# Kernel optimization log

Measured on AMD Instinct MI355X. Metric: run time of the kernel, lower is better.

## Reference

```python
import jax, jax.numpy as jnp
import numpy as np

B, SEQ, VOCAB, DIM, DEPTH, HEADS, DH, M, FF, LABELS = 4, 2048, 4096, 768, 6, 12, 64, 256, 3072, 2
INNER = HEADS * DH
EPS_K = 1e-4  # FAVOR+ kernel eps
EPS_LN = 1e-5


def setup_inputs() -> dict:
    key = jax.random.key(0)
    ks = jax.random.split(key, 16)
    g = lambda k, shape: (jax.random.normal(k, shape, jnp.float32) * 0.02)
    return {
        "x": jax.random.randint(ks[0], (B, SEQ), 0, VOCAB),
        "token_emb": g(ks[1], (VOCAB, DIM)),
        "pos_emb": g(ks[2], (SEQ, DIM)),
        "ln1_g": jnp.ones((DEPTH, DIM)), "ln1_b": jnp.zeros((DEPTH, DIM)),
        "Wq": g(ks[3], (DEPTH, DIM, INNER)),
        "Wk": g(ks[4], (DEPTH, DIM, INNER)),
        "Wv": g(ks[5], (DEPTH, DIM, INNER)),
        "Wo": g(ks[6], (DEPTH, INNER, DIM)), "bo": jnp.zeros((DEPTH, DIM)),
        "proj": jax.random.normal(ks[7], (DEPTH, M, DH), jnp.float32),  # FAVOR+ random projections (buffer)
        "ln2_g": jnp.ones((DEPTH, DIM)), "ln2_b": jnp.zeros((DEPTH, DIM)),
        "W1": g(ks[8], (DEPTH, DIM, FF)), "b1": jnp.zeros((DEPTH, FF)),
        "W2": g(ks[9], (DEPTH, FF, DIM)), "b2": jnp.zeros((DEPTH, DIM)),
        "lnf_g": jnp.ones((DIM,)), "lnf_b": jnp.zeros((DIM,)),
        "Wp": g(ks[10], (DIM, DIM)), "bp": jnp.zeros((DIM,)),
        "Wc": g(ks[11], (DIM, LABELS)), "bc": jnp.zeros((LABELS,)),
    }


def layernorm(x, g, b):
    mu = jnp.mean(x, -1, keepdims=True)
    var = jnp.mean(jnp.square(x - mu), -1, keepdims=True)
    return (x - mu) * jax.lax.rsqrt(var + EPS_LN) * g + b


def softmax_kernel(x, proj, is_query):
    # x: [b,h,n,d]  proj: [m,d]   (FAVOR+ positive softmax features)
    d = x.shape[-1]
    m = proj.shape[0]
    dn = d ** -0.25            # data normalizer 1/sqrt(sqrt(d))
    ratio = m ** -0.5
    xd = jnp.einsum('bhnd,md->bhnm', x * dn, proj)
    diag = 0.5 * jnp.sum(jnp.square(x), -1, keepdims=True) * (dn * dn)  # [b,h,n,1]
    if is_query:
        stab = jnp.max(xd, axis=-1, keepdims=True)
    else:
        stab = jnp.max(xd, axis=(-2, -1), keepdims=True)
    return ratio * (jnp.exp(xd - diag - stab) + EPS_K)


def favor_attention(y, Wq, Wk, Wv, Wo, bo, proj):
    b, n, _ = y.shape
    split = lambda t: t.reshape(b, n, HEADS, DH).transpose(0, 2, 1, 3)  # -> bhnd
    q, k, v = split(y @ Wq), split(y @ Wk), split(y @ Wv)
    qp = softmax_kernel(q, proj, True)    # [b,h,n,m]
    kp = softmax_kernel(k, proj, False)   # [b,h,n,m]
    k_sum = jnp.sum(kp, axis=2)                                  # [b,h,m]
    d_inv = 1.0 / jnp.einsum('bhnm,bhm->bhn', qp, k_sum)
    ctx = jnp.einsum('bhnm,bhnd->bhmd', kp, v)                   # [b,h,m,d]
    out = jnp.einsum('bhmd,bhnm,bhn->bhnd', ctx, qp, d_inv)
    out = out.transpose(0, 2, 1, 3).reshape(b, n, INNER)
    return out @ Wo + bo


def reference(x, token_emb, pos_emb, ln1_g, ln1_b, Wq, Wk, Wv, Wo, bo, proj,
              ln2_g, ln2_b, W1, b1, W2, b2, lnf_g, lnf_b, Wp, bp, Wc, bc):
    n = x.shape[1]
    h = token_emb[x] + pos_emb[None, :n]
    for l in range(DEPTH):
        h = h + favor_attention(layernorm(h, ln1_g[l], ln1_b[l]),
                                Wq[l], Wk[l], Wv[l], Wo[l], bo[l], proj[l])
        y = layernorm(h, ln2_g[l], ln2_b[l])
        h = h + (jax.nn.gelu(y @ W1[l] + b1[l], approximate=False) @ W2[l] + b2[l])
    h = layernorm(h, lnf_g, lnf_b)
    pooled = jnp.tanh(h[:, 0] @ Wp + bp)   # BertPooler on first token
    return pooled @ Wc + bc                 # [B, LABELS]
```

## Files before the change

kernel.cpp:

```cpp
#include <hip/hip_runtime.h>
#include <hip/hip_bf16.h>
#include <math.h>

#define B_ 4
#define SEQ_ 2048
#define DIM_ 768
#define DEPTH_ 6
#define HEADS_ 12
#define DH_ 64
#define MF_ 256
#define FF_ 3072
#define ROWS_ 8192
#define BH_ 48
#define QKVW_ 2304
#define DN_ 0.3535533905932738f
#define RATIO_ 0.0625f
#define EPSK_ 1e-4f
#define EPSLN_ 1e-5f

typedef unsigned short u16;
typedef unsigned int   u32;
typedef __bf16 bf16x8 __attribute__((ext_vector_type(8)));
typedef u16    u16x8  __attribute__((ext_vector_type(8)));
typedef float  f32x4  __attribute__((ext_vector_type(4)));

__device__ inline u16 f2bf(float x){
  u32 u = __builtin_bit_cast(u32, x);
  return (u16)((u + 0x7FFFu + ((u>>16)&1u)) >> 16);
}
__device__ inline float bf2f(u16 v){ return __builtin_bit_cast(float, (u32)v<<16); }

__device__ inline void gload16(const u16* g, u16* lds){
  __builtin_amdgcn_global_load_lds(
    (const __attribute__((address_space(1))) u32*)(const void*)g,
    (__attribute__((address_space(3))) u32*)(void*)lds, 16, 0, 0);
}

__global__ void embed_kernel(const int* __restrict__ x, const float4* __restrict__ tok,
                             const float4* __restrict__ pos, float4* __restrict__ h){
  const int C4 = DIM_/4;
  long total = (long)ROWS_*C4;
  for (long i = (long)blockIdx.x*blockDim.x + threadIdx.x; i < total;
       i += (long)gridDim.x*blockDim.x){
    int row = (int)(i / C4); int c = (int)(i - (long)row*C4);
    int n = row & (SEQ_-1);
    float4 a = tok[(long)x[row]*C4 + c];
    float4 p = pos[(long)n*C4 + c];
    float4 o; o.x=a.x+p.x; o.y=a.y+p.y; o.z=a.z+p.z; o.w=a.w+p.w;
    h[i] = o;
  }
}

__global__ __launch_bounds__(256) void ln_kernel(const float* __restrict__ X,
                          const float* __restrict__ g, const float* __restrict__ bta,
                          u16* __restrict__ Y){
  int row = blockIdx.x; int t = threadIdx.x;
  const float* xr = X + (long)row*DIM_;
  float v0 = xr[t], v1 = xr[t+256], v2 = xr[t+512];
  float s = v0+v1+v2;
  float ss = v0*v0+v1*v1+v2*v2;
  int lane = t&63, wid = t>>6;
  #pragma unroll
  for (int off=32; off; off>>=1){ s += __shfl_xor(s,off); ss += __shfl_xor(ss,off); }
  __shared__ float red[8];
  if (lane==0){ red[wid]=s; red[4+wid]=ss; }
  __syncthreads();
  s  = red[0]+red[1]+red[2]+red[3];
  ss = red[4]+red[5]+red[6]+red[7];
  float mu  = s*(1.0f/DIM_);
  float var = ss*(1.0f/DIM_) - mu*mu;
  float rs  = rsqrtf(var + EPSLN_);
  u16* yr = Y + (long)row*DIM_;
  yr[t]     = f2bf((v0-mu)*rs*g[t]     + bta[t]);
  yr[t+256] = f2bf((v1-mu)*rs*g[t+256] + bta[t+256]);
  yr[t+512] = f2bf((v2-mu)*rs*g[t+512] + bta[t+512]);
}

__global__ __launch_bounds__(256) void tconv_kernel(const float* __restrict__ W,
        u16* __restrict__ WT, int K, int N){
  __shared__ float tile[32][33];
  int n0 = blockIdx.x*32, k0 = blockIdx.y*32;
  int tx = threadIdx.x & 31, ty = threadIdx.x >> 5;
  #pragma unroll
  for (int i=0;i<32;i+=8) tile[ty+i][tx] = W[(long)(k0+ty+i)*N + n0+tx];
  __syncthreads();
  #pragma unroll
  for (int i=0;i<32;i+=8) WT[(long)(n0+ty+i)*K + k0+tx] = f2bf(tile[tx][ty+i]);
}

__global__ __launch_bounds__(256) void tconv4_kernel(const float* __restrict__ Wq,
        const float* __restrict__ Wk, const float* __restrict__ Wv,
        const float* __restrict__ Wo, u16* __restrict__ dst){
  __shared__ float tile[32][33];
  int z = blockIdx.z;
  const float* W = (z==0)?Wq:(z==1)?Wk:(z==2)?Wv:Wo;
  u16* WT = dst + (long)z*589824;
  int n0 = blockIdx.x*32, k0 = blockIdx.y*32;
  int tx = threadIdx.x & 31, ty = threadIdx.x >> 5;
  #pragma unroll
  for (int i=0;i<32;i+=8) tile[ty+i][tx] = W[(long)(k0+ty+i)*768 + n0+tx];
  __syncthreads();
  #pragma unroll
  for (int i=0;i<32;i+=8) WT[(long)(n0+ty+i)*768 + k0+tx] = f2bf(tile[tx][ty+i]);
}

template<int FM, int FN, int WM, int WN, int ACT, int CMODE, int BATCH>
__global__ __launch_bounds__(256) void mgemm(const u16* __restrict__ A,
     const u16* __restrict__ BT, const float* __restrict__ bias,
     void* __restrict__ Cv, const float* __restrict__ scale,
     int M, int N, int K, int ldC){
  (void)M;
  constexpr int BM = WM*FM*16, BN = WN*FN*16;
  constexpr int ACH = BM/16, BCH = BN/16;
  __shared__ u16 As[BM*32];
  __shared__ u16 Bs[BN*32];
  int tid = threadIdx.x; int w = tid>>6, l = tid&63;
  int bx, by;
  if (BATCH){ bx = blockIdx.x; by = blockIdx.y; }
  else {
    int bid = blockIdx.y*gridDim.x + blockIdx.x;
    int cpx = (gridDim.x*gridDim.y) >> 3;
    int swz = (bid & 7)*cpx + (bid >> 3);
    bx = swz % gridDim.x; by = swz / gridDim.x;
  }
  int m0 = by*BM, n0 = bx*BN;
  long coff = 0, srow0 = 0;
  if (BATCH){
    int z = blockIdx.z;
    A  += (long)z*2048*K;
    BT += (long)z*(long)N*K;
    coff  = (long)(z/HEADS_)*SEQ_*(long)ldC + (long)(z%HEADS_)*64;
    srow0 = (long)z*SEQ_;
  }
  f32x4 acc[FM][FN];
  #pragma unroll
  for (int i=0;i<FM;i++)
    #pragma unroll
    for (int j=0;j<FN;j++) acc[i][j] = (f32x4){0.f,0.f,0.f,0.f};

  const int row_l = l>>2, cq_l = l&3;
  const int wm = w / WN, wn = w % WN;
  const int kq = l>>4, rl15 = l&15;

  for (int k0=0; k0<K; k0+=32){
    __syncthreads();
    for (int c = w; c < ACH; c += 4){
      int r = c*16 + row_l;
      int gq = cq_l ^ ((r>>1)&3);
      gload16(A + (long)(m0+r)*K + k0 + gq*8, As + c*512);
    }
    for (int c = w; c < BCH; c += 4){
      int r = c*16 + row_l;
      int gq = cq_l ^ ((r>>1)&3);
      gload16(BT + (long)(n0+r)*K + k0 + gq*8, Bs + c*512);
    }
    __syncthreads();
    bf16x8 af[FM], bfr[FN];
    #pragma unroll
    for (int mi=0; mi<FM; mi++){
      int rr = (wm*FM + mi)*16 + rl15;
      int g = kq ^ ((rr>>1)&3);
      af[mi] = *(const bf16x8*)(As + rr*32 + g*8);
    }
    #pragma unroll
    for (int ni=0; ni<FN; ni++){
      int rr = (wn*FN + ni)*16 + rl15;
      int g = kq ^ ((rr>>1)&3);
      bfr[ni] = *(const bf16x8*)(Bs + rr*32 + g*8);
    }
    #pragma unroll
    for (int mi=0; mi<FM; mi++)
      #pragma unroll
      for (int ni=0; ni<FN; ni++)
        acc[mi][ni] = __builtin_amdgcn_mfma_f32_16x16x32_bf16(af[mi], bfr[ni], acc[mi][ni], 0, 0, 0);
  }

  int cc = l&15, rq = l>>4;
  #pragma unroll
  for (int mi=0; mi<FM; mi++){
    #pragma unroll
    for (int ni=0; ni<FN; ni++){
      int gcol = n0 + (wn*FN+ni)*16 + cc;
      float bv = bias ? bias[gcol] : 0.f;
      #pragma unroll
      for (int r4=0; r4<4; r4++){
        int grow = m0 + (wm*FM+mi)*16 + rq*4 + r4;
        float v = acc[mi][ni][r4] + bv;
        if (ACT) v = 0.5f*v*(1.0f + erff(v*0.70710678118654752f));
        if (CMODE==1){
          float* C = (float*)Cv;
          C[(long)grow*ldC + gcol] += v;
        } else if (CMODE==2){
          v *= scale[srow0 + grow];
          ((u16*)Cv)[coff + (long)grow*ldC + gcol] = f2bf(v);
        } else {
          ((u16*)Cv)[(long)grow*ldC + gcol] = f2bf(v);
        }
      }
    }
  }
}

__global__ void projcvt_kernel(const float* __restrict__ p, u16* __restrict__ hi,
                               u16* __restrict__ lo){
  int i = blockIdx.x*256 + threadIdx.x;
  float v = p[i];
  u16 h = f2bf(v);
  hi[i] = h;
  lo[i] = f2bf(v - bf2f(h));
}

__global__ __launch_bounds__(256) void diag2_kernel(const u16* __restrict__ qkvp,
        float* __restrict__ diagq, float* __restrict__ diagk){
  int chunk = blockIdx.x, z = blockIdx.y, which = blockIdx.z, t = threadIdx.x;
  const u16* X = qkvp + (which ? 768 : 0);
  float* outp = which ? diagk : diagq;
  int n = chunk*256 + t;
  const u16* r = X + ((long)(z/HEADS_)*SEQ_ + n)*QKVW_ + (z%HEADS_)*DH_;
  float s = 0.f;
  #pragma unroll
  for (int q=0;q<8;q++){
    u16x8 v = *(const u16x8*)(r + q*8);
    #pragma unroll
    for (int j=0;j<8;j++){ float f = bf2f(v[j]); s += f*f; }
  }
  outp[(long)z*SEQ_ + n] = 0.5f*DN_*DN_*s;
}

template<int MODE>
__global__ __launch_bounds__(256) void featgemm(const u16* __restrict__ X,
     const u16* __restrict__ PB, const float* __restrict__ diag,
     const float* __restrict__ stab, u16* __restrict__ kp,
     float* __restrict__ fmaxp){
  __shared__ u16 As[128*32];
  __shared__ u16 Bs[128*32];
  __shared__ float wred[4];
  int tid = threadIdx.x; int w = tid>>6, l = tid&63;
  int n0 = blockIdx.x*128, m0 = blockIdx.y*128;
  int z = blockIdx.z;
  const u16* A = X + (long)(z/HEADS_)*SEQ_*QKVW_ + (z%HEADS_)*DH_;
  f32x4 acc[4][4];
  #pragma unroll
  for (int i=0;i<4;i++)
    #pragma unroll
    for (int j=0;j<4;j++) acc[i][j] = (f32x4){0.f,0.f,0.f,0.f};
  const int row_l = l>>2, cq_l = l&3;
  const int wm = w>>1, wn = w&1;
  const int kq = l>>4, rl15 = l&15;

  for (int k0=0; k0<64; k0+=32){
    __syncthreads();
    for (int c = w; c < 8; c += 4){
      int r = c*16 + row_l;
      int gq = cq_l ^ ((r>>1)&3);
      gload16(A + (long)(m0+r)*QKVW_ + k0 + gq*8, As + c*512);
    }
    for (int c = w; c < 8; c += 4){
      int r = c*16 + row_l;
      int gq = cq_l ^ ((r>>1)&3);
      gload16(PB + (long)(n0+r)*64 + k0 + gq*8, Bs + c*512);
    }
    __syncthreads();
    bf16x8 af[4], bfr[4];
    #pragma unroll
    for (int mi=0; mi<4; mi++){
      int rr = (wm*4 + mi)*16 + rl15;
      int g = kq ^ ((rr>>1)&3);
      af[mi] = *(const bf16x8*)(As + rr*32 + g*8);
    }
    #pragma unroll
    for (int ni=0; ni<4; ni++){
      int rr = (wn*4 + ni)*16 + rl15;
      int g = kq ^ ((rr>>1)&3);
      bfr[ni] = *(const bf16x8*)(Bs + rr*32 + g*8);
    }
    #pragma unroll
    for (int mi=0; mi<4; mi++)
      #pragma unroll
      for (int ni=0; ni<4; ni++)
        acc[mi][ni] = __builtin_amdgcn_mfma_f32_16x16x32_bf16(af[mi], bfr[ni], acc[mi][ni], 0, 0, 0);
  }

  if (MODE==0){
    float bm = -1e30f;
    #pragma unroll
    for (int mi=0;mi<4;mi++)
      #pragma unroll
      for (int ni=0;ni<4;ni++)
        #pragma unroll
        for (int r4=0;r4<4;r4++) bm = fmaxf(bm, acc[mi][ni][r4]);
    bm *= DN_;
    #pragma unroll
    for (int off=32; off; off>>=1) bm = fmaxf(bm, __shfl_xor(bm,off));
    if (l==0) wred[w] = bm;
    __syncthreads();
    if (tid==0)
      fmaxp[z*32 + blockIdx.y*2 + blockIdx.x] =
        fmaxf(fmaxf(wred[0],wred[1]),fmaxf(wred[2],wred[3]));
  } else {
    float st = stab[z];
    int cc = l&15, rq = l>>4;
    #pragma unroll
    for (int mi=0; mi<4; mi++){
      #pragma unroll
      for (int ni=0; ni<4; ni++){
        int gcol = n0 + (wn*4+ni)*16 + cc;
        #pragma unroll
        for (int r4=0; r4<4; r4++){
          int grow = m0 + (wm*4+mi)*16 + rq*4 + r4;
          float v = acc[mi][ni][r4]*DN_;
          float e = RATIO_*(expf(v - diag[(long)z*SEQ_ + grow] - st) + EPSK_);
          kp[((long)z*SEQ_ + grow)*MF_ + gcol] = f2bf(e);
        }
      }
    }
  }
}

__global__ void fmax_reduce(const float* __restrict__ fmaxp, float* __restrict__ stab){
  int z = blockIdx.x, t = threadIdx.x;
  float m = (t<32) ? fmaxp[z*32+t] : -1e30f;
  #pragma unroll
  for (int off=32; off; off>>=1) m = fmaxf(m, __shfl_xor(m,off));
  if (t==0) stab[z] = m;
}

__global__ __launch_bounds__(256) void qfeatgemm(const u16* __restrict__ X,
     const u16* __restrict__ PH, const u16* __restrict__ PL,
     const float* __restrict__ diagq, const float* __restrict__ ksum,
     u16* __restrict__ qp, float* __restrict__ dinv){
  __shared__ u16 As[64*32];
  __shared__ u16 Bh[256*32];
  __shared__ u16 Bl[256*32];
  __shared__ float ksl[256];
  __shared__ float rmax[64][4];
  __shared__ float rsum[64][4];
  int tid = threadIdx.x; int w = tid>>6, l = tid&63;
  int n0 = blockIdx.x*64;
  int z = blockIdx.y;
  const u16* A = X + (long)(z/HEADS_)*SEQ_*QKVW_ + (z%HEADS_)*DH_;
  ksl[tid] = ksum[(long)z*MF_ + tid];
  f32x4 acc[4][4];
  #pragma unroll
  for (int i=0;i<4;i++)
    #pragma unroll
    for (int j=0;j<4;j++) acc[i][j] = (f32x4){0.f,0.f,0.f,0.f};
  const int row_l = l>>2, cq_l = l&3;
  const int kq = l>>4, rl15 = l&15;

  for (int k0=0; k0<64; k0+=32){
    __syncthreads();
    {
      int r = w*16 + row_l;
      int gq = cq_l ^ ((r>>1)&3);
      gload16(A + (long)(n0+r)*QKVW_ + k0 + gq*8, As + w*512);
    }
    for (int c = w; c < 16; c += 4){
      int r = c*16 + row_l;
      int gq = cq_l ^ ((r>>1)&3);
      gload16(PH + (long)r*64 + k0 + gq*8, Bh + c*512);
      gload16(PL + (long)r*64 + k0 + gq*8, Bl + c*512);
    }
    __syncthreads();
    bf16x8 af[4], bh[4], bl[4];
    #pragma unroll
    for (int mi=0; mi<4; mi++){
      int rr = mi*16 + rl15;
      int g = kq ^ ((rr>>1)&3);
      af[mi] = *(const bf16x8*)(As + rr*32 + g*8);
    }
    #pragma unroll
    for (int ni=0; ni<4; ni++){
      int rr = (w*4 + ni)*16 + rl15;
      int g = kq ^ ((rr>>1)&3);
      bh[ni] = *(const bf16x8*)(Bh + rr*32 + g*8);
      bl[ni] = *(const bf16x8*)(Bl + rr*32 + g*8);
    }
    #pragma unroll
    for (int mi=0; mi<4; mi++)
      #pragma unroll
      for (int ni=0; ni<4; ni++){
        acc[mi][ni] = __builtin_amdgcn_mfma_f32_16x16x32_bf16(af[mi], bh[ni], acc[mi][ni], 0, 0, 0);
        acc[mi][ni] = __builtin_amdgcn_mfma_f32_16x16x32_bf16(af[mi], bl[ni], acc[mi][ni], 0, 0, 0);
      }
  }

  int cc = l&15, rq = l>>4;
  #pragma unroll
  for (int mi=0; mi<4; mi++){
    #pragma unroll
    for (int r4=0; r4<4; r4++){
      float pm = fmaxf(fmaxf(acc[mi][0][r4],acc[mi][1][r4]),
                       fmaxf(acc[mi][2][r4],acc[mi][3][r4]));
      pm = fmaxf(pm, __shfl_xor(pm,1)); pm = fmaxf(pm, __shfl_xor(pm,2));
      pm = fmaxf(pm, __shfl_xor(pm,4)); pm = fmaxf(pm, __shfl_xor(pm,8));
      if (cc==0) rmax[mi*16 + rq*4 + r4][w] = pm;
    }
  }
  __syncthreads();
  #pragma unroll
  for (int mi=0; mi<4; mi++){
    #pragma unroll
    for (int r4=0; r4<4; r4++){
      int row = mi*16 + rq*4 + r4;
      float mx = fmaxf(fmaxf(rmax[row][0],rmax[row][1]),
                       fmaxf(rmax[row][2],rmax[row][3])) * DN_;
      float dq = diagq[(long)z*SEQ_ + n0 + row];
      float dv = 0.f;
      #pragma unroll
      for (int ni=0; ni<4; ni++){
        int col = w*64 + ni*16 + cc;
        float qpv = RATIO_*(expf(acc[mi][ni][r4]*DN_ - dq - mx) + EPSK_);
        u16 qb = f2bf(qpv);
        qp[((long)z*SEQ_ + n0 + row)*MF_ + col] = qb;
        dv += bf2f(qb)*ksl[col];
      }
      dv += __shfl_xor(dv,1); dv += __shfl_xor(dv,2);
      dv += __shfl_xor(dv,4); dv += __shfl_xor(dv,8);
      if (cc==0) rsum[row][w] = dv;
    }
  }
  __syncthreads();
  if (tid < 64){
    float s = rsum[tid][0]+rsum[tid][1]+rsum[tid][2]+rsum[tid][3];
    dinv[(long)z*SEQ_ + n0 + tid] = 1.0f/s;
  }
}

__global__ __launch_bounds__(256) void ctxgemm(const u16* __restrict__ qkv,
     const u16* __restrict__ kp, float* __restrict__ part){
  int kc = blockIdx.x;
  int z  = blockIdx.y;
  int b = z/HEADS_, hh = z%HEADS_;
  int tid = threadIdx.x; int w = tid>>6, l = tid&63;
  __shared__ u16 Vt[64*40];
  __shared__ u16 Kpt[256*40];
  f32x4 acc[4][4];
  #pragma unroll
  for (int i=0;i<4;i++)
    #pragma unroll
    for (int j=0;j<4;j++) acc[i][j] = (f32x4){0.f,0.f,0.f,0.f};
  int n_l = tid&31, grp = tid>>5;
  const int kq = l>>4, rl15 = l&15;
  const long vbase = (long)b*SEQ_*QKVW_ + hh*DH_ + 1536;
  const long kbase = (long)z*SEQ_*MF_;

  for (int s=0; s<32; s++){
    int nG = kc*1024 + s*32 + n_l;
    __syncthreads();
    {
      u16x8 v = *(const u16x8*)(qkv + vbase + (long)nG*QKVW_ + grp*8);
      #pragma unroll
      for (int j=0;j<8;j++) Vt[(grp*8+j)*40 + n_l] = v[j];
    }
    {
      const u16* src = kp + kbase + (long)nG*MF_ + grp*32;
      #pragma unroll
      for (int q=0;q<4;q++){
        u16x8 v = *(const u16x8*)(src + q*8);
        #pragma unroll
        for (int j=0;j<8;j++) Kpt[(grp*32+q*8+j)*40 + n_l] = v[j];
      }
    }
    __syncthreads();
    bf16x8 af[4], bfr[4];
    #pragma unroll
    for (int mi=0; mi<4; mi++)
      af[mi] = *(const bf16x8*)(Vt + (mi*16+rl15)*40 + kq*8);
    #pragma unroll
    for (int ni=0; ni<4; ni++)
      bfr[ni] = *(const bf16x8*)(Kpt + ((w*4+ni)*16+rl15)*40 + kq*8);
    #pragma unroll
    for (int mi=0; mi<4; mi++)
      #pragma unroll
      for (int ni=0; ni<4; ni++)
        acc[mi][ni] = __builtin_amdgcn_mfma_f32_16x16x32_bf16(af[mi], bfr[ni], acc[mi][ni], 0, 0, 0);
  }

  int cc = l&15, rq = l>>4;
  float* pb = part + ((long)kc*BH_ + z)*(64*MF_);
  #pragma unroll
  for (int mi=0; mi<4; mi++){
    #pragma unroll
    for (int ni=0; ni<4; ni++){
      int m = (w*4+ni)*16 + cc;
      #pragma unroll
      for (int r4=0; r4<4; r4++){
        int d = mi*16 + rq*4 + r4;
        pb[(long)d*MF_ + m] = acc[mi][ni][r4];
      }
    }
  }
}

__global__ void ctx_reduce2(const float* __restrict__ part, u16* __restrict__ ctxT){
  const long NT = (long)BH_*64*MF_;
  for (long i = (long)blockIdx.x*256 + threadIdx.x; i < NT; i += (long)gridDim.x*256){
    ctxT[i] = f2bf(part[i] + part[NT + i]);
  }
}

__global__ void ksum_part_kernel(const u16* __restrict__ kp, float* __restrict__ ksp){
  int kc = blockIdx.x, z = blockIdx.y, t = threadIdx.x;
  const u16* base = kp + ((long)z*SEQ_ + kc*256)*MF_ + t;
  float s = 0.f;
  for (int n=0;n<256;n++) s += bf2f(base[(long)n*MF_]);
  ksp[(z*8+kc)*MF_ + t] = s;
}

__global__ void ksum_reduce(const float* __restrict__ part, float* __restrict__ ksum){
  int z = blockIdx.x; int t = threadIdx.x;
  float s = 0.f;
  #pragma unroll
  for (int c=0;c<8;c++) s += part[(z*8+c)*MF_ + t];
  ksum[z*MF_+t] = s;
}

__global__ __launch_bounds__(256) void pooler_kernel(const float* __restrict__ h,
                           const float* __restrict__ g, const float* __restrict__ bta,
                           const float* __restrict__ Wp, const float* __restrict__ bp,
                           const float* __restrict__ Wc, const float* __restrict__ bc,
                           float* __restrict__ out){
  int b = blockIdx.x, t = threadIdx.x;
  __shared__ float xn[768];
  __shared__ float pl[768];
  __shared__ float red[8];
  const float* row = h + (long)b*SEQ_*DIM_;
  float v0=row[t], v1=row[t+256], v2=row[t+512];
  float s = v0+v1+v2, ss = v0*v0+v1*v1+v2*v2;
  int lane=t&63, wid=t>>6;
  #pragma unroll
  for (int off=32; off; off>>=1){ s += __shfl_xor(s,off); ss += __shfl_xor(ss,off); }
  if (lane==0){ red[wid]=s; red[4+wid]=ss; }
  __syncthreads();
  s  = red[0]+red[1]+red[2]+red[3];
  ss = red[4]+red[5]+red[6]+red[7];
  float mu = s*(1.0f/DIM_);
  float var = ss*(1.0f/DIM_) - mu*mu;
  float rs = rsqrtf(var + EPSLN_);
  xn[t]     = (v0-mu)*rs*g[t]     + bta[t];
  xn[t+256] = (v1-mu)*rs*g[t+256] + bta[t+256];
  xn[t+512] = (v2-mu)*rs*g[t+512] + bta[t+512];
  __syncthreads();
  #pragma unroll
  for (int jj=0;jj<3;jj++){
    int j = t + jj*256;
    float a = bp[j];
    for (int i=0;i<768;i++) a += xn[i]*Wp[(long)i*DIM_ + j];
    pl[j] = tanhf(a);
  }
  __syncthreads();
  if (wid < 2){
    float a = 0.f;
    for (int i=lane;i<768;i+=64) a += pl[i]*Wc[i*2+wid];
    #pragma unroll
    for (int off=32; off; off>>=1) a += __shfl_xor(a,off);
    if (lane==0) out[b*2+wid] = a + bc[wid];
  }
}

extern "C" void kernel_launch(void* const* d_in, const int* in_sizes, int n_in,
                              void* d_out, int out_size, void* d_ws, size_t ws_size,
                              hipStream_t stream) {
  (void)in_sizes; (void)n_in; (void)out_size; (void)ws_size;
  const int*   x    = (const int*)  d_in[0];
  const float* tok  = (const float*)d_in[1];
  const float* pos  = (const float*)d_in[2];
  const float* ln1g = (const float*)d_in[3];
  const float* ln1b = (const float*)d_in[4];
  const float* Wq   = (const float*)d_in[5];
  const float* Wk   = (const float*)d_in[6];
  const float* Wv   = (const float*)d_in[7];
  const float* Wo   = (const float*)d_in[8];
  const float* bo   = (const float*)d_in[9];
  const float* proj = (const float*)d_in[10];
  const float* ln2g = (const float*)d_in[11];
  const float* ln2b = (const float*)d_in[12];
  const float* W1   = (const float*)d_in[13];
  const float* b1   = (const float*)d_in[14];
  const float* W2   = (const float*)d_in[15];
  const float* b2   = (const float*)d_in[16];
  const float* lnfg = (const float*)d_in[17];
  const float* lnfb = (const float*)d_in[18];
  const float* Wp   = (const float*)d_in[19];
  const float* bp   = (const float*)d_in[20];
  const float* Wc   = (const float*)d_in[21];
  const float* bc   = (const float*)d_in[22];
  float* out = (float*)d_out;

  char* wsb = (char*)d_ws;
  float* h     = (float*)(wsb + 0);
  u16*   ybf   = (u16*)  (wsb + 25165824);
  float* ctxp2 = (float*)(wsb + 25165824);
  float* diag  = (float*)(wsb + 31457280);
  float* diagq = (float*)(wsb + 31850496);
  float* ksp   = (float*)(wsb + 32243712);
  float* fmaxp = (float*)(wsb + 32636928);
  u16*   projbf= (u16*)  (wsb + 32643072);
  u16*   projlo= (u16*)  (wsb + 32675840);
  float* stab  = (float*)(wsb + 32708608);
  u16*   qkv   = (u16*)  (wsb + 37748736);
  u16*   ffnbf = (u16*)  (wsb + 75497472);
  u16*   kp    = (u16*)  (wsb + 75497472);
  u16*   qp    = (u16*)  (wsb + 75497472);
  u16*   wT    = (u16*)  (wsb + 125829120);
  u16*   ctxT  = (u16*)  (wsb + 139984896);
  float* ksum  = (float*)(wsb + 141557760);
  float* dinv  = (float*)(wsb + 141606912);
  u16* attnbf  = ybf;

  u16* wtq = wT;
  u16* wto = wT + 1769472;
  u16* wt1 = wT + 2359296;
  u16* wt2 = wT + 4718592;
  (void)wto;

  embed_kernel<<<2048,256,0,stream>>>(x,(const float4*)tok,(const float4*)pos,(float4*)h);

  dim3 gD64(6, 128);
  dim3 gQKV(18, 64);
  dim3 gF(24, 64);
  dim3 gQ2(1, 16, BH_);
  dim3 gFG(2, 16, BH_);
  dim3 gQF(32, BH_);

  for (int l=0; l<DEPTH_; l++){
    const float* wq  = Wq + (size_t)l*DIM_*DIM_;
    const float* wk  = Wk + (size_t)l*DIM_*DIM_;
    const float* wv  = Wv + (size_t)l*DIM_*DIM_;
    const float* wo  = Wo + (size_t)l*DIM_*DIM_;
    const float* prj = proj + (size_t)l*MF_*DH_;
    const float* w1  = W1 + (size_t)l*DIM_*FF_;
    const float* w2  = W2 + (size_t)l*FF_*DIM_;

    tconv4_kernel<<<dim3(24,24,4),256,0,stream>>>(wq, wk, wv, wo, wtq);
    tconv_kernel<<<dim3(96,24),256,0,stream>>>(w1, wt1, 768, 3072);
    tconv_kernel<<<dim3(24,96),256,0,stream>>>(w2, wt2, 3072, 768);

    ln_kernel<<<ROWS_,256,0,stream>>>(h, ln1g+(size_t)l*DIM_, ln1b+(size_t)l*DIM_, ybf);
    mgemm<4,4,2,2,0,0,0><<<gQKV,256,0,stream>>>(ybf, wtq, nullptr, qkv, nullptr, ROWS_, QKVW_, 768, QKVW_);

    projcvt_kernel<<<64,256,0,stream>>>(prj, projbf, projlo);
    diag2_kernel<<<dim3(8,BH_,2),256,0,stream>>>(qkv, diagq, diag);
    featgemm<0><<<gFG,256,0,stream>>>(qkv + 768, projbf, nullptr, nullptr, nullptr, fmaxp);
    fmax_reduce<<<BH_,64,0,stream>>>(fmaxp, stab);
    featgemm<1><<<gFG,256,0,stream>>>(qkv + 768, projbf, diag, stab, kp, nullptr);
    ctxgemm<<<dim3(2,BH_),256,0,stream>>>(qkv, kp, ctxp2);
    ctx_reduce2<<<768,256,0,stream>>>(ctxp2, ctxT);
    ksum_part_kernel<<<dim3(8,BH_),256,0,stream>>>(kp, ksp);
    ksum_reduce<<<BH_,256,0,stream>>>(ksp, ksum);

    qfeatgemm<<<gQF,256,0,stream>>>(qkv, projbf, projlo, diagq, ksum, qp, dinv);
    mgemm<2,4,4,1,0,2,1><<<gQ2,256,0,stream>>>(qp, ctxT, nullptr, attnbf, dinv, SEQ_, 64, 256, 768);

    mgemm<2,4,2,2,0,1,0><<<gD64,256,0,stream>>>(attnbf, wto, bo+(size_t)l*DIM_, h, nullptr, ROWS_, 768, 768, 768);

    ln_kernel<<<ROWS_,256,0,stream>>>(h, ln2g+(size_t)l*DIM_, ln2b+(size_t)l*DIM_, ybf);
    mgemm<4,4,2,2,1,0,0><<<gF,256,0,stream>>>(ybf, wt1, b1+(size_t)l*FF_, ffnbf, nullptr, ROWS_, 3072, 768, 3072);
    mgemm<2,4,2,2,0,1,0><<<gD64,256,0,stream>>>(ffnbf, wt2, b2+(size_t)l*DIM_, h, nullptr, ROWS_, 768, 3072, 768);
  }

  pooler_kernel<<<B_,256,0,stream>>>(h, lnfg, lnfb, Wp, bp, Wc, bc, out);
}
```

Baseline: 2.496 ms.

## Fuse key-feature column sums into featgemm and parallelize pooler across blocks

The key-feature GEMM epilogue now accumulates per-column sums of the bf16-rounded kp values, reduces them through shared memory, and writes per-block partials. This removes the separate ksum_part pass that re-read all of kp from memory every layer. The final pooler is also split into a row layernorm kernel, a 48-block matrix-vector kernel and a small classifier kernel, replacing a 4-block kernel that did a serial 768x768 matvec. The cost is an extra shared buffer plus __syncthreads in featgemm, two extra launches at the end, and moved workspace offsets.

```diff
diff --git a/kernel.cpp b/kernel.cpp
--- a/kernel.cpp
+++ b/kernel.cpp
@@ -298,21 +298,33 @@
       fmaxp[z*32 + blockIdx.y*2 + blockIdx.x] =
         fmaxf(fmaxf(wred[0],wred[1]),fmaxf(wred[2],wred[3]));
   } else {
+    __shared__ float ksred[128][8];
     float st = stab[z];
     int cc = l&15, rq = l>>4;
     #pragma unroll
-    for (int mi=0; mi<4; mi++){
-      #pragma unroll
-      for (int ni=0; ni<4; ni++){
-        int gcol = n0 + (wn*4+ni)*16 + cc;
+    for (int ni=0; ni<4; ni++){
+      int gcol = n0 + (wn*4+ni)*16 + cc;
+      float cs = 0.f;
+      #pragma unroll
+      for (int mi=0; mi<4; mi++){
         #pragma unroll
         for (int r4=0; r4<4; r4++){
           int grow = m0 + (wm*4+mi)*16 + rq*4 + r4;
           float v = acc[mi][ni][r4]*DN_;
           float e = RATIO_*(expf(v - diag[(long)z*SEQ_ + grow] - st) + EPSK_);
-          kp[((long)z*SEQ_ + grow)*MF_ + gcol] = f2bf(e);
+          u16 eb = f2bf(e);
+          kp[((long)z*SEQ_ + grow)*MF_ + gcol] = eb;
+          cs += bf2f(eb);
         }
       }
+      ksred[(wn*4+ni)*16 + cc][wm*4 + rq] = cs;
+    }
+    __syncthreads();
+    if (tid < 128){
+      float s = 0.f;
+      #pragma unroll
+      for (int q=0;q<8;q++) s += ksred[tid][q];
+      fmaxp[((long)z*16 + blockIdx.y)*MF_ + n0 + tid] = s;
     }
   }
 }
@@ -323,6 +335,14 @@
   #pragma unroll
   for (int off=32; off; off>>=1) m = fmaxf(m, __shfl_xor(m,off));
   if (t==0) stab[z] = m;
+}
+
+__global__ void ksum_reduce(const float* __restrict__ part, float* __restrict__ ksum){
+  int z = blockIdx.x; int t = threadIdx.x;
+  float s = 0.f;
+  #pragma unroll
+  for (int c=0;c<16;c++) s += part[((long)z*16+c)*MF_ + t];
+  ksum[z*MF_+t] = s;
 }
 
 __global__ __launch_bounds__(256) void qfeatgemm(const u16* __restrict__ X,
@@ -500,37 +520,17 @@
   }
 }
 
-__global__ void ksum_part_kernel(const u16* __restrict__ kp, float* __restrict__ ksp){
-  int kc = blockIdx.x, z = blockIdx.y, t = threadIdx.x;
-  const u16* base = kp + ((long)z*SEQ_ + kc*256)*MF_ + t;
-  float s = 0.f;
-  for (int n=0;n<256;n++) s += bf2f(base[(long)n*MF_]);
-  ksp[(z*8+kc)*MF_ + t] = s;
-}
-
-__global__ void ksum_reduce(const float* __restrict__ part, float* __restrict__ ksum){
-  int z = blockIdx.x; int t = threadIdx.x;
-  float s = 0.f;
-  #pragma unroll
-  for (int c=0;c<8;c++) s += part[(z*8+c)*MF_ + t];
-  ksum[z*MF_+t] = s;
-}
-
-__global__ __launch_bounds__(256) void pooler_kernel(const float* __restrict__ h,
-                           const float* __restrict__ g, const float* __restrict__ bta,
-                           const float* __restrict__ Wp, const float* __restrict__ bp,
-                           const float* __restrict__ Wc, const float* __restrict__ bc,
-                           float* __restrict__ out){
-  int b = blockIdx.x, t = threadIdx.x;
-  __shared__ float xn[768];
-  __shared__ float pl[768];
-  __shared__ float red[8];
+__global__ __launch_bounds__(256) void lnrow0_kernel(const float* __restrict__ h,
+                          const float* __restrict__ g, const float* __restrict__ bta,
+                          float* __restrict__ xnf){
+  int b = blockIdx.x; int t = threadIdx.x;
   const float* row = h + (long)b*SEQ_*DIM_;
   float v0=row[t], v1=row[t+256], v2=row[t+512];
   float s = v0+v1+v2, ss = v0*v0+v1*v1+v2*v2;
   int lane=t&63, wid=t>>6;
   #pragma unroll
   for (int off=32; off; off>>=1){ s += __shfl_xor(s,off); ss += __shfl_xor(ss,off); }
+  __shared__ float red[8];
   if (lane==0){ red[wid]=s; red[4+wid]=ss; }
   __syncthreads();
   s  = red[0]+red[1]+red[2]+red[3];
@@ -538,25 +538,49 @@
   float mu = s*(1.0f/DIM_);
   float var = ss*(1.0f/DIM_) - mu*mu;
   float rs = rsqrtf(var + EPSLN_);
-  xn[t]     = (v0-mu)*rs*g[t]     + bta[t];
-  xn[t+256] = (v1-mu)*rs*g[t+256] + bta[t+256];
-  xn[t+512] = (v2-mu)*rs*g[t+512] + bta[t+512];
-  __syncthreads();
-  #pragma unroll
-  for (int jj=0;jj<3;jj++){
-    int j = t + jj*256;
-    float a = bp[j];
-    for (int i=0;i<768;i++) a += xn[i]*Wp[(long)i*DIM_ + j];
-    pl[j] = tanhf(a);
-  }
-  __syncthreads();
-  if (wid < 2){
-    float a = 0.f;
-    for (int i=lane;i<768;i+=64) a += pl[i]*Wc[i*2+wid];
-    #pragma unroll
-    for (int off=32; off; off>>=1) a += __shfl_xor(a,off);
-    if (lane==0) out[b*2+wid] = a + bc[wid];
-  }
+  float* xr = xnf + b*DIM_;
+  xr[t]     = (v0-mu)*rs*g[t]     + bta[t];
+  xr[t+256] = (v1-mu)*rs*g[t+256] + bta[t+256];
+  xr[t+512] = (v2-mu)*rs*g[t+512] + bta[t+512];
+}
+
+__global__ __launch_bounds__(256) void poolmv_kernel(const float* __restrict__ xnf,
+        const float* __restrict__ Wp, const float* __restrict__ bp,
+        float* __restrict__ pooled){
+  int c = blockIdx.x;
+  int b = blockIdx.y;
+  __shared__ float xs[768];
+  __shared__ float red[64][5];
+  int t = threadIdx.x;
+  xs[t] = xnf[b*DIM_+t]; xs[t+256] = xnf[b*DIM_+t+256]; xs[t+512] = xnf[b*DIM_+t+512];
+  __syncthreads();
+  int col_l = t & 63, seg = t >> 6;
+  int col = c*64 + col_l;
+  const float* wp = Wp + col;
+  float a = 0.f;
+  #pragma unroll 4
+  for (int i = seg*192; i < (seg+1)*192; i++) a += xs[i]*wp[(long)i*DIM_];
+  red[col_l][seg] = a;
+  __syncthreads();
+  if (t < 64){
+    float s = red[t][0]+red[t][1]+red[t][2]+red[t][3] + bp[c*64+t];
+    pooled[b*DIM_ + c*64 + t] = tanhf(s);
+  }
+}
+
+__global__ __launch_bounds__(256) void cls_kernel(const float* __restrict__ pooled,
+        const float* __restrict__ Wc, const float* __restrict__ bc,
+        float* __restrict__ out){
+  int t = threadIdx.x;
+  int b = t >> 6, lane = t & 63;
+  float a0 = 0.f, a1 = 0.f;
+  for (int i = lane; i < 768; i += 64){
+    float p = pooled[b*DIM_ + i];
+    a0 += p*Wc[i*2]; a1 += p*Wc[i*2+1];
+  }
+  #pragma unroll
+  for (int off=32; off; off>>=1){ a0 += __shfl_xor(a0,off); a1 += __shfl_xor(a1,off); }
+  if (lane==0){ out[b*2] = a0 + bc[0]; out[b*2+1] = a1 + bc[1]; }
 }
 
 extern "C" void kernel_launch(void* const* d_in, const int* in_sizes, int n_in,
@@ -595,10 +619,12 @@
   float* diag  = (float*)(wsb + 31457280);
   float* diagq = (float*)(wsb + 31850496);
   float* ksp   = (float*)(wsb + 32243712);
-  float* fmaxp = (float*)(wsb + 32636928);
-  u16*   projbf= (u16*)  (wsb + 32643072);
-  u16*   projlo= (u16*)  (wsb + 32675840);
-  float* stab  = (float*)(wsb + 32708608);
+  float* fmaxp = (float*)(wsb + 33030144);
+  u16*   projbf= (u16*)  (wsb + 33036288);
+  u16*   projlo= (u16*)  (wsb + 33069056);
+  float* stab  = (float*)(wsb + 33101824);
+  float* xnf   = (float*)(wsb + 25165824);
+  float* pooled= (float*)(wsb + 25178112);
   u16*   qkv   = (u16*)  (wsb + 37748736);
   u16*   ffnbf = (u16*)  (wsb + 75497472);
   u16*   kp    = (u16*)  (wsb + 75497472);
@@ -613,7 +639,6 @@
   u16* wto = wT + 1769472;
   u16* wt1 = wT + 2359296;
   u16* wt2 = wT + 4718592;
-  (void)wto;
 
   embed_kernel<<<2048,256,0,stream>>>(x,(const float4*)tok,(const float4*)pos,(float4*)h);
 
@@ -644,10 +669,9 @@
     diag2_kernel<<<dim3(8,BH_,2),256,0,stream>>>(qkv, diagq, diag);
     featgemm<0><<<gFG,256,0,stream>>>(qkv + 768, projbf, nullptr, nullptr, nullptr, fmaxp);
     fmax_reduce<<<BH_,64,0,stream>>>(fmaxp, stab);
-    featgemm<1><<<gFG,256,0,stream>>>(qkv + 768, projbf, diag, stab, kp, nullptr);
+    featgemm<1><<<gFG,256,0,stream>>>(qkv + 768, projbf, diag, stab, kp, ksp);
     ctxgemm<<<dim3(2,BH_),256,0,stream>>>(qkv, kp, ctxp2);
     ctx_reduce2<<<768,256,0,stream>>>(ctxp2, ctxT);
-    ksum_part_kernel<<<dim3(8,BH_),256,0,stream>>>(kp, ksp);
     ksum_reduce<<<BH_,256,0,stream>>>(ksp, ksum);
 
     qfeatgemm<<<gQF,256,0,stream>>>(qkv, projbf, projlo, diagq, ksum, qp, dinv);
@@ -660,5 +684,7 @@
     mgemm<2,4,2,2,0,1,0><<<gD64,256,0,stream>>>(ffnbf, wt2, b2+(size_t)l*DIM_, h, nullptr, ROWS_, 768, 3072, 768);
   }
 
-  pooler_kernel<<<B_,256,0,stream>>>(h, lnfg, lnfb, Wp, bp, Wc, bc, out);
-}
+  lnrow0_kernel<<<B_,256,0,stream>>>(h, lnfg, lnfb, xnf);
+  poolmv_kernel<<<dim3(12,B_),256,0,stream>>>(xnf, Wp, bp, pooled);
+  cls_kernel<<<1,256,0,stream>>>(pooled, Wc, bc, out);
+}
```

Measured after the change: 2.411 ms. 3.4% less time.
